# Kernel optimization log

Hardware: AMD Instinct MI355X
Metric: run time of the kernel (lower is better)

Reference implementation:

```python
import jax, jax.numpy as jnp
import numpy as np

B_SZ = 64            # oft_block_size
IN_F = 4096
OUT_F = 4096
R_IN = IN_F // B_SZ   # 64 blocks
R_OUT = OUT_F // B_SZ # 64 blocks
N_TRI = B_SZ * (B_SZ - 1) // 2  # 2016 packed strict-upper entries
NUM_NEUMANN = 5

_rows, _cols = np.triu_indices(B_SZ, k=1)
ROWS = jnp.asarray(_rows, dtype=jnp.int32)
COLS = jnp.asarray(_cols, dtype=jnp.int32)


def setup_inputs() -> dict:
    key = jax.random.key(0)
    k = jax.random.split(key, 5)
    x = jax.random.normal(k[0], (4, 2048, IN_F), dtype=jnp.float32)
    # small skew entries so the Neumann series approximates the Cayley transform
    Ro = jax.random.normal(k[1], (R_OUT, N_TRI), dtype=jnp.float32) * 0.01
    Ri = jax.random.normal(k[2], (R_IN, N_TRI), dtype=jnp.float32) * 0.01
    W = jax.random.normal(k[3], (OUT_F, IN_F), dtype=jnp.float32) * (1.0 / np.sqrt(IN_F))
    bias = jax.random.normal(k[4], (OUT_F,), dtype=jnp.float32) * 0.01
    rng = np.random.default_rng(0)
    perm_in = rng.permutation(IN_F)
    perm_in_inv = np.argsort(perm_in)
    perm_out = rng.permutation(OUT_F)
    return {
        "x": x, "Ro": Ro, "Ri": Ri, "W": W, "bias": bias,
        "perm_in_inv": jnp.asarray(perm_in_inv, dtype=jnp.int32),
        "perm_out": jnp.asarray(perm_out, dtype=jnp.int32),
    }


def _skew(vec):
    # vec: (r, n_tri) packed strict-upper entries -> (r, b, b) skew-symmetric
    r = vec.shape[0]
    M = jnp.zeros((r, B_SZ, B_SZ), dtype=vec.dtype).at[:, ROWS, COLS].set(vec)
    return M - jnp.swapaxes(M, -2, -1)


def _cayley_neumann(Q):
    # R = I + 2*(Q + Q^2 + Q^3 + Q^4)   (num_neumann_terms = 5)
    I = jnp.eye(B_SZ, dtype=Q.dtype)
    acc = Q
    Qp = Q
    for _ in range(3, NUM_NEUMANN):
        pass
    Q2 = jnp.matmul(Q, Q)
    acc = acc + Q2
    Qp = Q2
    for _ in range(3, NUM_NEUMANN):
        Qp = jnp.matmul(Qp, Q)
        acc = acc + Qp
    return I + 2.0 * acc


def reference(x, Ro, Ri, W, bias, perm_in_inv, perm_out):
    R_out = _cayley_neumann(_skew(Ro))   # (r_out, b, b)
    R_in = _cayley_neumann(_skew(Ri))    # (r_in, b, b)

    B, S, _ = x.shape
    xp = x[..., perm_in_inv]                               # input permutation
    xb = xp.reshape(B, S, R_IN, B_SZ)
    xR = jnp.einsum('bsrc,rcd->bsrd', xb, R_in)            # block-diag right rotate
    y = xR.reshape(B, S, IN_F) @ W.T + bias                # base linear
    yb = y.reshape(B, S, R_OUT, B_SZ)
    yR = jnp.einsum('bsrc,rcd->bsrd', yb, R_out)           # block-diag output rotate
    out = yR.reshape(B, S, OUT_F)[..., perm_out]           # output permutation
    return out
```

## Files before the change

### kernel.cpp

```cpp
#include <hip/hip_runtime.h>
#include <stdint.h>

#define IN_F 4096
#define OUT_F 4096
#define NTRI 2016

typedef unsigned short u16;
typedef __attribute__((ext_vector_type(8))) short short8;
typedef __attribute__((ext_vector_type(4))) float f32x4;
typedef __attribute__((ext_vector_type(4))) unsigned short u16x4;

__device__ __forceinline__ u16 f2bf(float f) {
    uint32_t u = __builtin_bit_cast(uint32_t, f);
    u = (u + 0x7FFFu + ((u >> 16) & 1u)) >> 16;
    return (u16)u;
}

__device__ __forceinline__ void gload16(const void* g, void* l) {
    __builtin_amdgcn_global_load_lds((__attribute__((address_space(1))) void*)g,
                                     (__attribute__((address_space(3))) void*)l,
                                     16, 0, 0);
}

__global__ void k_inv_perm(const int* __restrict__ perm_in_inv, int* __restrict__ pin) {
    int i = blockIdx.x * 256 + threadIdx.x;
    if (i < IN_F) pin[perm_in_inv[i]] = i;
}

__global__ __launch_bounds__(256) void k_cayley(const float* __restrict__ Ro,
                                                const float* __restrict__ Ri,
                                                float* __restrict__ Rout,
                                                float* __restrict__ RinT) {
    __shared__ __align__(16) float Qs[64 * 64];
    __shared__ __align__(16) float Ps[64 * 68];
    __shared__ __align__(16) float Ts[64 * 68];
    int b = blockIdx.x;
    const float* vec = (b < 64) ? (Ro + (size_t)b * NTRI) : (Ri + (size_t)(b - 64) * NTRI);
    int t = threadIdx.x;
    int tr = t >> 4, tc = t & 15;
#pragma unroll
    for (int e = 0; e < 16; ++e) {
        int el = e * 256 + t;
        int i = el >> 6, j = el & 63;
        float q = 0.f;
        if (i < j) q =  vec[i * 63 - (i * (i - 1)) / 2 + (j - i - 1)];
        if (i > j) q = -vec[j * 63 - (j * (j - 1)) / 2 + (i - j - 1)];
        Qs[el] = q;
    }
    __syncthreads();
    float a2[4][4], a3[4][4], a4[4][4];
#pragma unroll
    for (int i = 0; i < 4; ++i)
#pragma unroll
        for (int j = 0; j < 4; ++j) { a2[i][j] = 0.f; a3[i][j] = 0.f; a4[i][j] = 0.f; }
    for (int k = 0; k < 64; ++k) {
        f32x4 qa = *(const f32x4*)&Qs[k * 64 + tr * 4];
        f32x4 qb = *(const f32x4*)&Qs[k * 64 + tc * 4];
#pragma unroll
        for (int i = 0; i < 4; ++i)
#pragma unroll
            for (int j = 0; j < 4; ++j) a2[i][j] -= qa[i] * qb[j];
    }
#pragma unroll
    for (int i = 0; i < 4; ++i)
#pragma unroll
        for (int j = 0; j < 4; ++j) Ps[(tr * 4 + i) * 68 + tc * 4 + j] = a2[i][j];
    __syncthreads();
    for (int k = 0; k < 64; ++k) {
        f32x4 pa = *(const f32x4*)&Ps[k * 68 + tr * 4];
        f32x4 qb = *(const f32x4*)&Qs[k * 64 + tc * 4];
#pragma unroll
        for (int i = 0; i < 4; ++i)
#pragma unroll
            for (int j = 0; j < 4; ++j) a3[i][j] += pa[i] * qb[j];
    }
#pragma unroll
    for (int i = 0; i < 4; ++i)
#pragma unroll
        for (int j = 0; j < 4; ++j) Ts[(tc * 4 + j) * 68 + tr * 4 + i] = -a3[i][j];
    __syncthreads();
    for (int k = 0; k < 64; ++k) {
        f32x4 ta = *(const f32x4*)&Ts[k * 68 + tr * 4];
        f32x4 qb = *(const f32x4*)&Qs[k * 64 + tc * 4];
#pragma unroll
        for (int i = 0; i < 4; ++i)
#pragma unroll
            for (int j = 0; j < 4; ++j) a4[i][j] -= ta[i] * qb[j];
    }
    if (b < 64) {
        float* dst = Rout + (size_t)b * 4096;
#pragma unroll
        for (int i = 0; i < 4; ++i) {
            int gi = tr * 4 + i;
            f32x4 q4 = *(const f32x4*)&Qs[gi * 64 + tc * 4];
            f32x4 o;
#pragma unroll
            for (int j = 0; j < 4; ++j) {
                int gj = tc * 4 + j;
                float v = 2.f * (q4[j] + a2[i][j] + a3[i][j] + a4[i][j]) + ((gi == gj) ? 1.f : 0.f);
                o[j] = v;
            }
            *(f32x4*)&dst[gi * 64 + tc * 4] = o;
        }
    } else {
        float* dstT = RinT + (size_t)(b - 64) * 4096;
#pragma unroll
        for (int i = 0; i < 4; ++i) {
            int gi = tr * 4 + i;
            f32x4 q4 = *(const f32x4*)&Qs[gi * 64 + tc * 4];
#pragma unroll
            for (int j = 0; j < 4; ++j) {
                int gj = tc * 4 + j;
                float v = 2.f * (q4[j] + a2[i][j] + a3[i][j] + a4[i][j]) + ((gi == gj) ? 1.f : 0.f);
                dstT[gj * 64 + gi] = v;
            }
        }
    }
}

__global__ void k_bias_rot(const float* __restrict__ bias, const float* __restrict__ Rout,
                           float* __restrict__ bias_prime) {
    int r = blockIdx.x;
    int d = threadIdx.x;
    const float* Rb = Rout + (size_t)r * 4096;
    float s = 0.f;
    for (int c = 0; c < 64; ++c) s += bias[r * 64 + c] * Rb[c * 64 + d];
    bias_prime[r * 64 + d] = s;
}

__global__ __launch_bounds__(256) void k_fold(const float* __restrict__ W,
                                              const float* __restrict__ RinT,
                                              const float* __restrict__ Rout,
                                              u16* __restrict__ Ct) {
    __shared__ __align__(16) float Wb[64 * 64];
    __shared__ __align__(16) float RoS[64 * 64];
    __shared__ __align__(16) float RiTs[64 * 64];
    __shared__ __align__(16) float UdT[64 * 68];
    int s = blockIdx.x;
    int r = blockIdx.y;
    int t = threadIdx.x;
    int tr = t >> 4, tc = t & 15;
#pragma unroll
    for (int e = 0; e < 16; ++e) {
        int el = e * 256 + t;
        int hi = el >> 6, lo = el & 63;
        Wb[el]   = W[(size_t)(r * 64 + hi) * IN_F + s * 64 + lo];
        RoS[el]  = Rout[(size_t)r * 4096 + el];
        RiTs[el] = RinT[(size_t)s * 4096 + el];
    }
    __syncthreads();
    float a1[4][4];
#pragma unroll
    for (int i = 0; i < 4; ++i)
#pragma unroll
        for (int j = 0; j < 4; ++j) a1[i][j] = 0.f;
    for (int c = 0; c < 64; ++c) {
        f32x4 ro = *(const f32x4*)&RoS[c * 64 + tr * 4];
        f32x4 wb = *(const f32x4*)&Wb[c * 64 + tc * 4];
#pragma unroll
        for (int i = 0; i < 4; ++i)
#pragma unroll
            for (int j = 0; j < 4; ++j) a1[i][j] += ro[i] * wb[j];
    }
#pragma unroll
    for (int i = 0; i < 4; ++i)
#pragma unroll
        for (int j = 0; j < 4; ++j) UdT[(tc * 4 + j) * 68 + tr * 4 + i] = a1[i][j];
    __syncthreads();
    float a2[4][4];
#pragma unroll
    for (int i = 0; i < 4; ++i)
#pragma unroll
        for (int j = 0; j < 4; ++j) a2[i][j] = 0.f;
    for (int b = 0; b < 64; ++b) {
        f32x4 ri = *(const f32x4*)&RiTs[b * 64 + tc * 4];
        f32x4 ud = *(const f32x4*)&UdT[b * 68 + tr * 4];
#pragma unroll
        for (int ai = 0; ai < 4; ++ai)
#pragma unroll
            for (int dj = 0; dj < 4; ++dj) a2[ai][dj] += ri[ai] * ud[dj];
    }
#pragma unroll
    for (int dj = 0; dj < 4; ++dj) {
        u16x4 o;
#pragma unroll
        for (int ai = 0; ai < 4; ++ai) o[ai] = f2bf(a2[ai][dj]);
        *(u16x4*)&Ct[(size_t)(r * 64 + tr * 4 + dj) * IN_F + s * 64 + tc * 4] = o;
    }
}

__global__ __launch_bounds__(256) void k_permM(const u16* __restrict__ Ct,
                                               const int* __restrict__ pout,
                                               const int* __restrict__ pin,
                                               u16* __restrict__ Mt) {
    __shared__ u16 row[4096];
    int j = blockIdx.x;
    int t = threadIdx.x;
    const u16* sr = Ct + (size_t)pout[j] * IN_F;
#pragma unroll
    for (int e = 0; e < 16; ++e) row[e * 256 + t] = sr[e * 256 + t];
    __syncthreads();
    u16* dr = Mt + (size_t)j * IN_F;
#pragma unroll
    for (int e = 0; e < 16; ++e) {
        int k = e * 256 + t;
        dr[k] = row[pin[k]];
    }
}

__global__ void k_bias_perm(const float* __restrict__ bias_prime, const int* __restrict__ pout,
                            float* __restrict__ bias_final) {
    int j = blockIdx.x * 256 + threadIdx.x;
    if (j < OUT_F) bias_final[j] = bias_prime[pout[j]];
}

__global__ __launch_bounds__(256) void k_xcast(const float* __restrict__ x,
                                               u16* __restrict__ xb) {
    size_t idx = ((size_t)blockIdx.x * 256 + threadIdx.x) * 8;
    const f32x4* xp = (const f32x4*)(x + idx);
    f32x4 a = xp[0], b = xp[1];
    union { short8 v; u16 s[8]; } o;
    o.s[0] = f2bf(a[0]); o.s[1] = f2bf(a[1]); o.s[2] = f2bf(a[2]); o.s[3] = f2bf(a[3]);
    o.s[4] = f2bf(b[0]); o.s[5] = f2bf(b[1]); o.s[6] = f2bf(b[2]); o.s[7] = f2bf(b[3]);
    *(short8*)(xb + idx) = o.v;
}

__global__ __launch_bounds__(512, 2) void k_gemm(const u16* __restrict__ A,
                                                 const u16* __restrict__ Bt,
                                                 const float* __restrict__ bias,
                                                 float* __restrict__ out) {
    __shared__ __align__(16) u16 lds[65536];
    const int t = threadIdx.x;
    const int lane = t & 63;
    const int wid = t >> 6;
    const int wr = wid >> 2, wc = wid & 3;

    int flat = blockIdx.y * gridDim.x + blockIdx.x;
    int swz  = (flat & 7) * 64 + (flat >> 3);
    int bm = swz >> 4;
    int bn = swz & 15;

    const int srow = t >> 2;
    const int sks  = (t & 3) ^ ((t >> 3) & 3);
    const u16* sA0 = A  + (size_t)(bm * 256 + srow) * IN_F + sks * 8;
    const u16* sA1 = sA0 + (size_t)128 * IN_F;
    const u16* sB0 = Bt + (size_t)(bn * 256 + srow) * IN_F + sks * 8;
    const u16* sB1 = sB0 + (size_t)128 * IN_F;
    u16* dA = lds + t * 8;
    u16* dB = lds + 8192 + t * 8;

    const int frow = lane & 15;
    const int kg = lane >> 4;
    const int swzr = kg ^ ((frow >> 1) & 3);
    const int aoff = (wr * 128 + frow) * 32 + swzr * 8;
    const int boff = 8192 + (wc * 64 + frow) * 32 + swzr * 8;

    f32x4 acc[8][4];
#pragma unroll
    for (int m = 0; m < 8; ++m)
#pragma unroll
        for (int n = 0; n < 4; ++n) acc[m][n] = f32x4{0.f, 0.f, 0.f, 0.f};

#pragma unroll
    for (int p = 0; p < 3; ++p) {
        int off = p * 32;
        int bb = p * 16384;
        gload16(sA0 + off, dA + bb); gload16(sA1 + off, dA + bb + 4096);
        gload16(sB0 + off, dB + bb); gload16(sB1 + off, dB + bb + 4096);
    }
    asm volatile("s_waitcnt vmcnt(8)" ::: "memory");
    __builtin_amdgcn_s_barrier();

    for (int t4 = 0; t4 < 128; t4 += 4) {
#pragma unroll
        for (int u = 0; u < 4; ++u) {
            const int kt = t4 + u;
            const u16* base = lds + u * 16384;
            short8 af[8], bf[4];
            const u16* pa = base + aoff;
            const u16* pb = base + boff;
#pragma unroll
            for (int m = 0; m < 8; ++m) af[m] = *(const short8*)(pa + m * 512);
#pragma unroll
            for (int n = 0; n < 4; ++n) bf[n] = *(const short8*)(pb + n * 512);
            {
                int ts = kt + 3;
                int tsc = ts < 128 ? ts : 124;
                int off = tsc * 32;
                int bb = ((kt + 3) & 3) * 16384;
                gload16(sA0 + off, dA + bb); gload16(sA1 + off, dA + bb + 4096);
                gload16(sB0 + off, dB + bb); gload16(sB1 + off, dB + bb + 4096);
            }
            __builtin_amdgcn_s_setprio(1);
#pragma unroll
            for (int m = 0; m < 8; ++m)
#pragma unroll
                for (int n = 0; n < 4; ++n)
                    acc[m][n] = __builtin_amdgcn_mfma_f32_16x16x32_bf16(af[m], bf[n], acc[m][n], 0, 0, 0);
            __builtin_amdgcn_s_setprio(0);
            asm volatile("s_waitcnt vmcnt(8)" ::: "memory");
            __builtin_amdgcn_s_barrier();
        }
    }
    asm volatile("s_waitcnt vmcnt(0)" ::: "memory");

    const int col0 = bn * 256 + wc * 64 + frow;
    const int row0 = bm * 256 + wr * 128 + kg * 4;
    float bv[4];
#pragma unroll
    for (int n = 0; n < 4; ++n) bv[n] = bias[col0 + n * 16];
#pragma unroll
    for (int m = 0; m < 8; ++m)
#pragma unroll
        for (int n = 0; n < 4; ++n)
#pragma unroll
            for (int i = 0; i < 4; ++i)
                out[(size_t)(row0 + m * 16 + i) * OUT_F + col0 + n * 16] = acc[m][n][i] + bv[n];
}

extern "C" void kernel_launch(void* const* d_in, const int* in_sizes, int n_in,
                              void* d_out, int out_size, void* d_ws, size_t ws_size,
                              hipStream_t stream) {
    (void)in_sizes; (void)n_in; (void)out_size; (void)ws_size;
    const float* x    = (const float*)d_in[0];
    const float* Ro   = (const float*)d_in[1];
    const float* Ri   = (const float*)d_in[2];
    const float* W    = (const float*)d_in[3];
    const float* bias = (const float*)d_in[4];
    const int* perm_in_inv = (const int*)d_in[5];
    const int* perm_out    = (const int*)d_in[6];
    float* out = (float*)d_out;

    char* ws = (char*)d_ws;
    float* Rout   = (float*)(ws);
    float* RinT   = (float*)(ws + (1ull << 20));
    int*   pin    = (int*)(ws + (2ull << 20));
    float* bprime = (float*)(ws + (2ull << 20) + (1 << 16));
    float* bfinal = (float*)(ws + (2ull << 20) + (2 << 16));
    u16*   Mt     = (u16*)(ws + (4ull << 20));
    u16*   Ct     = (u16*)(ws + (36ull << 20));
    u16*   xb     = (u16*)(ws + (36ull << 20));

    k_inv_perm<<<16, 256, 0, stream>>>(perm_in_inv, pin);
    k_cayley<<<128, 256, 0, stream>>>(Ro, Ri, Rout, RinT);
    k_bias_rot<<<64, 64, 0, stream>>>(bias, Rout, bprime);
    k_fold<<<dim3(64, 64), 256, 0, stream>>>(W, RinT, Rout, Ct);
    k_permM<<<4096, 256, 0, stream>>>(Ct, perm_out, pin, Mt);
    k_bias_perm<<<16, 256, 0, stream>>>(bprime, perm_out, bfinal);
    k_xcast<<<16384, 256, 0, stream>>>(x, xb);
    k_gemm<<<dim3(16, 32), 512, 0, stream>>>(xb, Mt, bfinal, out);
}
```

Baseline: 369.3 us.

## Fold weights with bf16 MFMA, scatter output permutation, split GEMM loop phases

Result: faster. 333.9 us (-9.6%).

```diff
diff --git a/kernel.cpp b/kernel.cpp
--- a/kernel.cpp
+++ b/kernel.cpp
@@ -22,15 +22,23 @@
                                      16, 0, 0);
 }
 
-__global__ void k_inv_perm(const int* __restrict__ perm_in_inv, int* __restrict__ pin) {
+#define FENCE() asm volatile("" ::: "memory")
+
+__global__ void k_inv_perm(const int* __restrict__ perm_in_inv,
+                           const int* __restrict__ perm_out,
+                           int* __restrict__ pin, int* __restrict__ pinv_out) {
     int i = blockIdx.x * 256 + threadIdx.x;
-    if (i < IN_F) pin[perm_in_inv[i]] = i;
+    if (i < IN_F) {
+        pin[perm_in_inv[i]] = i;
+        pinv_out[perm_out[i]] = i;
+    }
 }
 
 __global__ __launch_bounds__(256) void k_cayley(const float* __restrict__ Ro,
                                                 const float* __restrict__ Ri,
                                                 float* __restrict__ Rout,
-                                                float* __restrict__ RinT) {
+                                                u16* __restrict__ QT16,
+                                                u16* __restrict__ P16) {
     __shared__ __align__(16) float Qs[64 * 64];
     __shared__ __align__(16) float Ps[64 * 68];
     __shared__ __align__(16) float Ts[64 * 68];
@@ -89,6 +97,7 @@
     }
     if (b < 64) {
         float* dst = Rout + (size_t)b * 4096;
+        u16* qt = QT16 + (size_t)b * 4096;
 #pragma unroll
         for (int i = 0; i < 4; ++i) {
             int gi = tr * 4 + i;
@@ -97,23 +106,26 @@
 #pragma unroll
             for (int j = 0; j < 4; ++j) {
                 int gj = tc * 4 + j;
-                float v = 2.f * (q4[j] + a2[i][j] + a3[i][j] + a4[i][j]) + ((gi == gj) ? 1.f : 0.f);
-                o[j] = v;
+                o[j] = 2.f * (q4[j] + a2[i][j] + a3[i][j] + a4[i][j]) + ((gi == gj) ? 1.f : 0.f);
             }
             *(f32x4*)&dst[gi * 64 + tc * 4] = o;
+#pragma unroll
+            for (int j = 0; j < 4; ++j) qt[(tc * 4 + j) * 64 + gi] = f2bf(o[j]);
         }
     } else {
-        float* dstT = RinT + (size_t)(b - 64) * 4096;
+        u16* p = P16 + (size_t)(b - 64) * 4096;
 #pragma unroll
         for (int i = 0; i < 4; ++i) {
             int gi = tr * 4 + i;
             f32x4 q4 = *(const f32x4*)&Qs[gi * 64 + tc * 4];
+            u16x4 pk;
 #pragma unroll
             for (int j = 0; j < 4; ++j) {
                 int gj = tc * 4 + j;
                 float v = 2.f * (q4[j] + a2[i][j] + a3[i][j] + a4[i][j]) + ((gi == gj) ? 1.f : 0.f);
-                dstT[gj * 64 + gi] = v;
+                pk[j] = f2bf(v);
             }
+            *(u16x4*)&p[gi * 64 + tc * 4] = pk;
         }
     }
 }
@@ -129,74 +141,118 @@
 }
 
 __global__ __launch_bounds__(256) void k_fold(const float* __restrict__ W,
-                                              const float* __restrict__ RinT,
-                                              const float* __restrict__ Rout,
-                                              u16* __restrict__ Ct) {
-    __shared__ __align__(16) float Wb[64 * 64];
-    __shared__ __align__(16) float RoS[64 * 64];
-    __shared__ __align__(16) float RiTs[64 * 64];
-    __shared__ __align__(16) float UdT[64 * 68];
-    int s = blockIdx.x;
-    int r = blockIdx.y;
-    int t = threadIdx.x;
-    int tr = t >> 4, tc = t & 15;
-#pragma unroll
-    for (int e = 0; e < 16; ++e) {
-        int el = e * 256 + t;
-        int hi = el >> 6, lo = el & 63;
-        Wb[el]   = W[(size_t)(r * 64 + hi) * IN_F + s * 64 + lo];
-        RoS[el]  = Rout[(size_t)r * 4096 + el];
-        RiTs[el] = RinT[(size_t)s * 4096 + el];
-    }
-    __syncthreads();
-    float a1[4][4];
-#pragma unroll
-    for (int i = 0; i < 4; ++i)
-#pragma unroll
-        for (int j = 0; j < 4; ++j) a1[i][j] = 0.f;
-    for (int c = 0; c < 64; ++c) {
-        f32x4 ro = *(const f32x4*)&RoS[c * 64 + tr * 4];
-        f32x4 wb = *(const f32x4*)&Wb[c * 64 + tc * 4];
-#pragma unroll
-        for (int i = 0; i < 4; ++i)
-#pragma unroll
-            for (int j = 0; j < 4; ++j) a1[i][j] += ro[i] * wb[j];
-    }
-#pragma unroll
-    for (int i = 0; i < 4; ++i)
-#pragma unroll
-        for (int j = 0; j < 4; ++j) UdT[(tc * 4 + j) * 68 + tr * 4 + i] = a1[i][j];
-    __syncthreads();
-    float a2[4][4];
-#pragma unroll
-    for (int i = 0; i < 4; ++i)
-#pragma unroll
-        for (int j = 0; j < 4; ++j) a2[i][j] = 0.f;
-    for (int b = 0; b < 64; ++b) {
-        f32x4 ri = *(const f32x4*)&RiTs[b * 64 + tc * 4];
-        f32x4 ud = *(const f32x4*)&UdT[b * 68 + tr * 4];
-#pragma unroll
-        for (int ai = 0; ai < 4; ++ai)
-#pragma unroll
-            for (int dj = 0; dj < 4; ++dj) a2[ai][dj] += ri[ai] * ud[dj];
-    }
-#pragma unroll
-    for (int dj = 0; dj < 4; ++dj) {
-        u16x4 o;
-#pragma unroll
-        for (int ai = 0; ai < 4; ++ai) o[ai] = f2bf(a2[ai][dj]);
-        *(u16x4*)&Ct[(size_t)(r * 64 + tr * 4 + dj) * IN_F + s * 64 + tc * 4] = o;
-    }
-}
-
-__global__ __launch_bounds__(256) void k_permM(const u16* __restrict__ Ct,
-                                               const int* __restrict__ pout,
+                                              const u16* __restrict__ P16,
+                                              const u16* __restrict__ QT16,
+                                              const int* __restrict__ pinv_out,
+                                              u16* __restrict__ Ctp) {
+    __shared__ __align__(16) u16 Wst[128 * 64];
+    __shared__ __align__(16) u16 Ut[64 * 128];
+    const int s = blockIdx.x;
+    const int br = blockIdx.y;
+    const int t = threadIdx.x;
+    const int lane = t & 63;
+    const int w = t >> 6;
+    const int fl = lane & 15;
+    const int kg = lane >> 4;
+
+    short8 bfP[4][2];
+    const u16* Pbase = P16 + (size_t)s * 4096;
+#pragma unroll
+    for (int nf = 0; nf < 4; ++nf)
+#pragma unroll
+        for (int kk = 0; kk < 2; ++kk)
+            bfP[nf][kk] = *(const short8*)(Pbase + (nf * 16 + fl) * 64 + kk * 32 + kg * 8);
+
+#pragma unroll
+    for (int q = 0; q < 4; ++q) {
+        int ci = q * 256 + t;
+        int row = ci >> 3, slot = ci & 7;
+        const float* src = W + (size_t)(br * 128 + row) * IN_F + s * 64 + slot * 8;
+        f32x4 v0 = *(const f32x4*)src;
+        f32x4 v1 = *(const f32x4*)(src + 4);
+        union { short8 v; u16 e[8]; } cv;
+        cv.e[0] = f2bf(v0[0]); cv.e[1] = f2bf(v0[1]); cv.e[2] = f2bf(v0[2]); cv.e[3] = f2bf(v0[3]);
+        cv.e[4] = f2bf(v1[0]); cv.e[5] = f2bf(v1[1]); cv.e[6] = f2bf(v1[2]); cv.e[7] = f2bf(v1[3]);
+        *(short8*)&Wst[row * 64 + (slot ^ (row & 7)) * 8] = cv.v;
+    }
+    __syncthreads();
+
+    f32x4 acc1[2][4];
+#pragma unroll
+    for (int mf = 0; mf < 2; ++mf)
+#pragma unroll
+        for (int nf = 0; nf < 4; ++nf) acc1[mf][nf] = f32x4{0.f, 0.f, 0.f, 0.f};
+#pragma unroll
+    for (int mf = 0; mf < 2; ++mf) {
+        int row = w * 32 + mf * 16 + fl;
+#pragma unroll
+        for (int kk = 0; kk < 2; ++kk) {
+            short8 a = *(const short8*)&Wst[row * 64 + ((kk * 4 + kg) ^ (row & 7)) * 8];
+#pragma unroll
+            for (int nf = 0; nf < 4; ++nf)
+                acc1[mf][nf] = __builtin_amdgcn_mfma_f32_16x16x32_bf16(a, bfP[nf][kk], acc1[mf][nf], 0, 0, 0);
+        }
+    }
+#pragma unroll
+    for (int mf = 0; mf < 2; ++mf)
+#pragma unroll
+        for (int nf = 0; nf < 4; ++nf) {
+            int i = nf * 16 + fl;
+            int c = w * 32 + mf * 16 + kg * 4;
+            u16x4 pk;
+#pragma unroll
+            for (int reg = 0; reg < 4; ++reg) pk[reg] = f2bf(acc1[mf][nf][reg]);
+            int slot = c >> 3, half = (c >> 2) & 1;
+            *(u16x4*)&Ut[i * 128 + ((slot ^ (i & 7)) << 3) + (half << 2)] = pk;
+        }
+    __syncthreads();
+
+    const int rbl = w >> 1;
+    const int r_g = br * 2 + rbl;
+    short8 aQ[2][2];
+#pragma unroll
+    for (int mf2 = 0; mf2 < 2; ++mf2) {
+        int d = (w & 1) * 32 + mf2 * 16 + fl;
+#pragma unroll
+        for (int kk = 0; kk < 2; ++kk)
+            aQ[mf2][kk] = *(const short8*)(QT16 + (size_t)r_g * 4096 + d * 64 + kk * 32 + kg * 8);
+    }
+    f32x4 acc2[2][4];
+#pragma unroll
+    for (int mf2 = 0; mf2 < 2; ++mf2)
+#pragma unroll
+        for (int nf = 0; nf < 4; ++nf) acc2[mf2][nf] = f32x4{0.f, 0.f, 0.f, 0.f};
+#pragma unroll
+    for (int kk = 0; kk < 2; ++kk)
+#pragma unroll
+        for (int nf = 0; nf < 4; ++nf) {
+            int i = nf * 16 + fl;
+            int slot = rbl * 8 + kk * 4 + kg;
+            short8 bu = *(const short8*)&Ut[i * 128 + ((slot ^ (i & 7)) << 3)];
+#pragma unroll
+            for (int mf2 = 0; mf2 < 2; ++mf2)
+                acc2[mf2][nf] = __builtin_amdgcn_mfma_f32_16x16x32_bf16(aQ[mf2][kk], bu, acc2[mf2][nf], 0, 0, 0);
+        }
+#pragma unroll
+    for (int mf2 = 0; mf2 < 2; ++mf2)
+#pragma unroll
+        for (int reg = 0; reg < 4; ++reg) {
+            int o_g = br * 128 + w * 32 + mf2 * 16 + kg * 4 + reg;
+            int j = pinv_out[o_g];
+            u16* dst = Ctp + (size_t)j * IN_F + s * 64;
+#pragma unroll
+            for (int nf = 0; nf < 4; ++nf)
+                dst[nf * 16 + fl] = f2bf(acc2[mf2][nf][reg]);
+        }
+}
+
+__global__ __launch_bounds__(256) void k_permM(const u16* __restrict__ Ctp,
                                                const int* __restrict__ pin,
                                                u16* __restrict__ Mt) {
     __shared__ u16 row[4096];
     int j = blockIdx.x;
     int t = threadIdx.x;
-    const u16* sr = Ct + (size_t)pout[j] * IN_F;
+    const u16* sr = Ctp + (size_t)j * IN_F;
 #pragma unroll
     for (int e = 0; e < 16; ++e) row[e * 256 + t] = sr[e * 256 + t];
     __syncthreads();
@@ -270,36 +326,54 @@
     }
     asm volatile("s_waitcnt vmcnt(8)" ::: "memory");
     __builtin_amdgcn_s_barrier();
+    FENCE();
 
     for (int t4 = 0; t4 < 128; t4 += 4) {
 #pragma unroll
         for (int u = 0; u < 4; ++u) {
             const int kt = t4 + u;
-            const u16* base = lds + u * 16384;
-            short8 af[8], bf[4];
-            const u16* pa = base + aoff;
-            const u16* pb = base + boff;
-#pragma unroll
-            for (int m = 0; m < 8; ++m) af[m] = *(const short8*)(pa + m * 512);
-#pragma unroll
-            for (int n = 0; n < 4; ++n) bf[n] = *(const short8*)(pb + n * 512);
-            {
-                int ts = kt + 3;
-                int tsc = ts < 128 ? ts : 124;
-                int off = tsc * 32;
-                int bb = ((kt + 3) & 3) * 16384;
-                gload16(sA0 + off, dA + bb); gload16(sA1 + off, dA + bb + 4096);
-                gload16(sB0 + off, dB + bb); gload16(sB1 + off, dB + bb + 4096);
-            }
+            const u16* pa = lds + u * 16384 + aoff;
+            const u16* pb = lds + u * 16384 + boff;
+            int ts = kt + 3;
+            int tsc = ts < 128 ? ts : 124;
+            int off = tsc * 32;
+            int bb = ((kt + 3) & 3) * 16384;
+            short8 af0[4], bfr[4];
+#pragma unroll
+            for (int m = 0; m < 4; ++m) af0[m] = *(const short8*)(pa + m * 512);
+#pragma unroll
+            for (int n = 0; n < 4; ++n) bfr[n] = *(const short8*)(pb + n * 512);
+            gload16(sA0 + off, dA + bb); gload16(sA1 + off, dA + bb + 4096);
+            FENCE();
+            __builtin_amdgcn_s_barrier();
+            FENCE();
             __builtin_amdgcn_s_setprio(1);
 #pragma unroll
-            for (int m = 0; m < 8; ++m)
+            for (int m = 0; m < 4; ++m)
 #pragma unroll
                 for (int n = 0; n < 4; ++n)
-                    acc[m][n] = __builtin_amdgcn_mfma_f32_16x16x32_bf16(af[m], bf[n], acc[m][n], 0, 0, 0);
+                    acc[m][n] = __builtin_amdgcn_mfma_f32_16x16x32_bf16(af0[m], bfr[n], acc[m][n], 0, 0, 0);
+            __builtin_amdgcn_s_setprio(0);
+            FENCE();
+            __builtin_amdgcn_s_barrier();
+            FENCE();
+            short8 af1[4];
+#pragma unroll
+            for (int m = 0; m < 4; ++m) af1[m] = *(const short8*)(pa + (m + 4) * 512);
+            gload16(sB0 + off, dB + bb); gload16(sB1 + off, dB + bb + 4096);
+            FENCE();
+            __builtin_amdgcn_s_barrier();
+            FENCE();
+            __builtin_amdgcn_s_setprio(1);
+#pragma unroll
+            for (int m = 0; m < 4; ++m)
+#pragma unroll
+                for (int n = 0; n < 4; ++n)
+                    acc[m + 4][n] = __builtin_amdgcn_mfma_f32_16x16x32_bf16(af1[m], bfr[n], acc[m + 4][n], 0, 0, 0);
             __builtin_amdgcn_s_setprio(0);
             asm volatile("s_waitcnt vmcnt(8)" ::: "memory");
             __builtin_amdgcn_s_barrier();
+            FENCE();
         }
     }
     asm volatile("s_waitcnt vmcnt(0)" ::: "memory");
@@ -333,19 +407,21 @@
 
     char* ws = (char*)d_ws;
     float* Rout   = (float*)(ws);
-    float* RinT   = (float*)(ws + (1ull << 20));
+    u16*   P16    = (u16*)(ws + (1ull << 20));
+    u16*   QT16   = (u16*)(ws + (1ull << 20) + (1 << 19));
     int*   pin    = (int*)(ws + (2ull << 20));
-    float* bprime = (float*)(ws + (2ull << 20) + (1 << 16));
-    float* bfinal = (float*)(ws + (2ull << 20) + (2 << 16));
+    int*   pinvo  = (int*)(ws + (2ull << 20) + (1 << 16));
+    float* bprime = (float*)(ws + (2ull << 20) + (2 << 16));
+    float* bfinal = (float*)(ws + (2ull << 20) + (3 << 16));
     u16*   Mt     = (u16*)(ws + (4ull << 20));
-    u16*   Ct     = (u16*)(ws + (36ull << 20));
     u16*   xb     = (u16*)(ws + (36ull << 20));
-
-    k_inv_perm<<<16, 256, 0, stream>>>(perm_in_inv, pin);
-    k_cayley<<<128, 256, 0, stream>>>(Ro, Ri, Rout, RinT);
+    u16*   Ctp    = (u16*)(ws + (36ull << 20));
+
+    k_inv_perm<<<16, 256, 0, stream>>>(perm_in_inv, perm_out, pin, pinvo);
+    k_cayley<<<128, 256, 0, stream>>>(Ro, Ri, Rout, QT16, P16);
     k_bias_rot<<<64, 64, 0, stream>>>(bias, Rout, bprime);
-    k_fold<<<dim3(64, 64), 256, 0, stream>>>(W, RinT, Rout, Ct);
-    k_permM<<<4096, 256, 0, stream>>>(Ct, perm_out, pin, Mt);
+    k_fold<<<dim3(64, 32), 256, 0, stream>>>(W, P16, QT16, pinvo, Ctp);
+    k_permM<<<4096, 256, 0, stream>>>(Ctp, pin, Mt);
     k_bias_perm<<<16, 256, 0, stream>>>(bprime, perm_out, bfinal);
     k_xcast<<<16384, 256, 0, stream>>>(x, xb);
     k_gemm<<<dim3(16, 32), 512, 0, stream>>>(xb, Mt, bfinal, out);
```
